# Optimization experiments

Measured on AMD Instinct MI355X. Metric: run time of the kernel, lower is better.

## Reference

```python
import jax, jax.numpy as jnp
import numpy as np

N, E = 8192, 262144
IN_DIM, OUT_DIM = 256, 256


def setup_inputs() -> dict:
    key = jax.random.key(0)
    k = jax.random.split(key, 7)
    x = jax.random.normal(k[0], (N, IN_DIM), dtype=jnp.float32)
    edge_index = jax.random.randint(k[1], (2, E), 0, N, dtype=jnp.int64)
    # parameters (nn.Linear stores weight as (out, in); bias=False everywhere)
    W = jax.random.normal(k[2], (OUT_DIM, IN_DIM), dtype=jnp.float32) / np.sqrt(IN_DIM)
    a_src = jax.random.normal(k[3], (OUT_DIM,), dtype=jnp.float32) / np.sqrt(OUT_DIM)
    a_dst = jax.random.normal(k[4], (OUT_DIM,), dtype=jnp.float32) / np.sqrt(OUT_DIM)
    gamma = jnp.ones((OUT_DIM,), dtype=jnp.float32)
    beta = jnp.zeros((OUT_DIM,), dtype=jnp.float32)
    return {"x": x, "edge_index": edge_index, "W": W, "a_src": a_src,
            "a_dst": a_dst, "gamma": gamma, "beta": beta}


def reference(x, edge_index, W, a_src, a_dst, gamma, beta):
    h = x @ W.T                                     # (N, D)
    src, dst = edge_index[0], edge_index[1]
    s_src = h @ a_src                               # (N,) attn_src logits
    s_dst = h @ a_dst                               # (N,)
    e = jax.nn.leaky_relu(s_src[src] + s_dst[dst], negative_slope=0.2)  # (E,)
    n = x.shape[0]
    # dense scatter: attn[dst, src] = e (duplicate edges overwrite, like torch)
    attn = jnp.zeros((n, n), dtype=x.dtype).at[dst, src].set(e)
    attn = jax.nn.softmax(attn + (attn == 0).astype(x.dtype) * -1e9, axis=-1)
    attn = attn * (attn > 1e-6).astype(x.dtype)
    out = attn @ h                                  # (N, D)
    z = jax.nn.elu(out) + h
    # LayerNorm (eps=1e-5, biased variance, matching torch)
    mean = jnp.mean(z, axis=-1, keepdims=True)
    var = jnp.var(z, axis=-1, keepdims=True)
    return gamma * (z - mean) * jax.lax.rsqrt(var + 1e-5) + beta
```

## Files before the change

kernel.cpp:

```cpp
#include <hip/hip_runtime.h>
#include <math.h>

#define N_NODES 8192
#define EDGES   262144
#define D       256
#define ROWCAP  128

typedef __attribute__((ext_vector_type(8))) short bf8;
typedef __attribute__((ext_vector_type(4))) float f32x4;


__device__ __forceinline__ ushort f2bf(float f) {
  unsigned u = __float_as_uint(f);
  return (ushort)((u + 0x7FFF + ((u >> 16) & 1)) >> 16);
}
__device__ __forceinline__ float bf2f(ushort s) {
  return __uint_as_float((unsigned)s << 16);
}

#define XQ 524288
#define WQ 16384
__global__ __launch_bounds__(256)
void split_kernel(const float* __restrict__ x, const float* __restrict__ W,
                  ushort* __restrict__ xhi, ushort* __restrict__ xlo,
                  ushort* __restrict__ whi, ushort* __restrict__ wlo) {
  int i = blockIdx.x * 256 + threadIdx.x;
  const float4* src; ushort *dh, *dl; int j;
  if (i < XQ) { src = (const float4*)x; dh = xhi; dl = xlo; j = i; }
  else        { src = (const float4*)W; dh = whi; dl = wlo; j = i - XQ; }
  float4 v = src[j];
  ushort4 h4, l4;
  h4.x = f2bf(v.x); l4.x = f2bf(v.x - bf2f(h4.x));
  h4.y = f2bf(v.y); l4.y = f2bf(v.y - bf2f(h4.y));
  h4.z = f2bf(v.z); l4.z = f2bf(v.z - bf2f(h4.z));
  h4.w = f2bf(v.w); l4.w = f2bf(v.w - bf2f(h4.w));
  *reinterpret_cast<ushort4*>(dh + (size_t)j * 4) = h4;
  *reinterpret_cast<ushort4*>(dl + (size_t)j * 4) = l4;
}

__global__ __launch_bounds__(256)
void gemm_mfma(const ushort* __restrict__ xhi, const ushort* __restrict__ xlo,
               const ushort* __restrict__ whi, const ushort* __restrict__ wlo,
               const float* __restrict__ a_src, const float* __restrict__ a_dst,
               float* __restrict__ h, float* __restrict__ s_src,
               float* __restrict__ s_dst) {
  const int wv = threadIdx.x >> 6, lane = threadIdx.x & 63;
  const int bm = blockIdx.x * 64 + wv * 16;
  const int bj = blockIdx.y * 64;
  const int r = lane & 15, kg = lane >> 4;
  const f32x4 z4 = {0.f, 0.f, 0.f, 0.f};
  f32x4 acc[4] = {z4, z4, z4, z4};
  const size_t arow = (size_t)(bm + r) * D;
  for (int k0 = 0; k0 < D; k0 += 32) {
    const int ko = k0 + kg * 8;
    bf8 ahi = *reinterpret_cast<const bf8*>(xhi + arow + ko);
    bf8 alo = *reinterpret_cast<const bf8*>(xlo + arow + ko);
#pragma unroll
    for (int ct = 0; ct < 4; ++ct) {
      const size_t boff = (size_t)(bj + ct * 16 + r) * D + ko;
      bf8 bhi = *reinterpret_cast<const bf8*>(whi + boff);
      bf8 blo = *reinterpret_cast<const bf8*>(wlo + boff);
      acc[ct] = __builtin_amdgcn_mfma_f32_16x16x32_bf16(ahi, bhi, acc[ct], 0, 0, 0);
      acc[ct] = __builtin_amdgcn_mfma_f32_16x16x32_bf16(ahi, blo, acc[ct], 0, 0, 0);
      acc[ct] = __builtin_amdgcn_mfma_f32_16x16x32_bf16(alo, bhi, acc[ct], 0, 0, 0);
    }
  }
  float pS[4] = {0.f, 0.f, 0.f, 0.f}, pD[4] = {0.f, 0.f, 0.f, 0.f};
#pragma unroll
  for (int ct = 0; ct < 4; ++ct) {
    const int col = bj + ct * 16 + r;
    const float av = a_src[col], dv = a_dst[col];
#pragma unroll
    for (int reg = 0; reg < 4; ++reg) {
      const float c = acc[ct][reg];
      h[(size_t)(bm + kg * 4 + reg) * D + col] = c;
      pS[reg] = fmaf(c, av, pS[reg]);
      pD[reg] = fmaf(c, dv, pD[reg]);
    }
  }
#pragma unroll
  for (int reg = 0; reg < 4; ++reg) {
    float ps = pS[reg], pd = pD[reg];
#pragma unroll
    for (int off = 1; off < 16; off <<= 1) {
      ps += __shfl_xor(ps, off, 64);
      pd += __shfl_xor(pd, off, 64);
    }
    if (r == 0) {
      atomicAdd(&s_src[bm + kg * 4 + reg], ps);
      atomicAdd(&s_dst[bm + kg * 4 + reg], pd);
    }
  }
}

__global__ __launch_bounds__(256)
void scatter_kernel(const int* __restrict__ ei, int* __restrict__ fill,
                    int* __restrict__ csr) {
  int lane = threadIdx.x & 63;
  unsigned long long b = __ballot(ei[lane * 2 + 1] == 0);
  int is64 = (b == 0xFFFFFFFFFFFFFFFFull) ? 1 : 0;
  int e = blockIdx.x * 256 + threadIdx.x;
  int src, dst;
  if (is64) { src = ei[2 * e];  dst = ei[2 * (EDGES + e)]; }
  else      { src = ei[e];      dst = ei[EDGES + e]; }
  int p = atomicAdd(&fill[dst], 1);
  if (p < ROWCAP) csr[dst * ROWCAP + p] = src;
}

__global__ __launch_bounds__(256)
void row_fused(const float* __restrict__ h, const float* __restrict__ s_src,
               const float* __restrict__ s_dst, const int* __restrict__ fill,
               const int* __restrict__ csr, const float* __restrict__ gamma,
               const float* __restrict__ beta, float* __restrict__ out) {
  __shared__ int   s_idx[4][ROWCAP];
  __shared__ float s_w[4][ROWCAP];
  const int w    = threadIdx.x >> 6;
  const int lane = threadIdx.x & 63;
  const int row  = blockIdx.x * 4 + w;
  int len = fill[row];
  if (len > ROWCAP) len = ROWCAP;
  const int len_pad = (len + 7) & ~7;
  const float sd = s_dst[row];

  for (int i = lane; i < len; i += 64) s_idx[w][i] = csr[row * ROWCAP + i];
  __syncthreads();

  float lmax = -3.0e38f;
  for (int i = lane; i < len; i += 64) {
    int s = s_idx[w][i];
    bool dup = false;
    for (int j = 0; j < i; ++j)
      if (s_idx[w][j] == s) { dup = true; break; }
    float v;
    if (dup) {
      v = -3.0e38f;
    } else {
      v = s_src[s] + sd;
      v = (v >= 0.f) ? v : 0.2f * v;
      if (v == 0.0f) v = -3.0e38f;
    }
    s_w[w][i] = v;
    lmax = fmaxf(lmax, v);
  }
#pragma unroll
  for (int off = 32; off; off >>= 1) lmax = fmaxf(lmax, __shfl_xor(lmax, off, 64));

  float lsum = 0.f;
  for (int i = lane; i < len; i += 64) {
    float e = expf(s_w[w][i] - lmax);
    s_w[w][i] = e;
    lsum += e;
  }
#pragma unroll
  for (int off = 32; off; off >>= 1) lsum += __shfl_xor(lsum, off, 64);
  float inv = (lsum > 0.f) ? (1.0f / lsum) : 0.f;
  for (int i = lane; i < len; i += 64) {
    float ww = s_w[w][i] * inv;
    s_w[w][i] = (ww > 1e-6f) ? ww : 0.f;
  }
  for (int i = len + lane; i < len_pad; i += 64) { s_w[w][i] = 0.f; s_idx[w][i] = 0; }
  __syncthreads();

  float4 acc = make_float4(0.f, 0.f, 0.f, 0.f);
  for (int i = 0; i < len_pad; i += 8) {
    float wg[8]; float4 hv[8];
#pragma unroll
    for (int u = 0; u < 8; ++u) {
      wg[u] = s_w[w][i + u];
      hv[u] = *reinterpret_cast<const float4*>(&h[(size_t)s_idx[w][i + u] * D + lane * 4]);
    }
#pragma unroll
    for (int u = 0; u < 8; ++u) {
      acc.x = fmaf(wg[u], hv[u].x, acc.x);
      acc.y = fmaf(wg[u], hv[u].y, acc.y);
      acc.z = fmaf(wg[u], hv[u].z, acc.z);
      acc.w = fmaf(wg[u], hv[u].w, acc.w);
    }
  }

  const float4 hr = *reinterpret_cast<const float4*>(&h[(size_t)row * D + lane * 4]);
  float4 z;
  z.x = ((acc.x > 0.f) ? acc.x : expm1f(acc.x)) + hr.x;
  z.y = ((acc.y > 0.f) ? acc.y : expm1f(acc.y)) + hr.y;
  z.z = ((acc.z > 0.f) ? acc.z : expm1f(acc.z)) + hr.z;
  z.w = ((acc.w > 0.f) ? acc.w : expm1f(acc.w)) + hr.w;

  float s1 = z.x + z.y + z.z + z.w;
#pragma unroll
  for (int off = 32; off; off >>= 1) s1 += __shfl_xor(s1, off, 64);
  float mean = s1 * (1.0f / 256.0f);
  float dx = z.x - mean, dy = z.y - mean, dz = z.z - mean, dw = z.w - mean;
  float s2 = dx * dx + dy * dy + dz * dz + dw * dw;
#pragma unroll
  for (int off = 32; off; off >>= 1) s2 += __shfl_xor(s2, off, 64);
  float rs = rsqrtf(s2 * (1.0f / 256.0f) + 1e-5f);

  const float4 gm = *reinterpret_cast<const float4*>(&gamma[lane * 4]);
  const float4 bt = *reinterpret_cast<const float4*>(&beta[lane * 4]);
  float4 o;
  o.x = gm.x * dx * rs + bt.x;
  o.y = gm.y * dy * rs + bt.y;
  o.z = gm.z * dz * rs + bt.z;
  o.w = gm.w * dw * rs + bt.w;
  *reinterpret_cast<float4*>(&out[(size_t)row * D + lane * 4]) = o;
}

extern "C" void kernel_launch(void* const* d_in, const int* in_sizes, int n_in,
                              void* d_out, int out_size, void* d_ws, size_t ws_size,
                              hipStream_t stream) {
  const float* x     = (const float*)d_in[0];
  const int*   ei    = (const int*)d_in[1];
  const float* W     = (const float*)d_in[2];
  const float* a_src = (const float*)d_in[3];
  const float* a_dst = (const float*)d_in[4];
  const float* gamma = (const float*)d_in[5];
  const float* beta  = (const float*)d_in[6];
  float* out = (float*)d_out;

  char* ws = (char*)d_ws;
  int*    fill  = (int*)(ws);
  float*  s_src = (float*)(ws + 32768);
  float*  s_dst = (float*)(ws + 65536);
  int*    csr   = (int*)(ws + 98304);
  float*  h     = (float*)(ws + 4292608);
  ushort* xhi   = (ushort*)(ws + 12681216);
  ushort* xlo   = (ushort*)(ws + 16875520);
  ushort* whi   = (ushort*)(ws + 21069824);
  ushort* wlo   = (ushort*)(ws + 21200896);
  if (ws_size < 21331968) return;

  hipMemsetAsync(ws, 0, 98304, stream);
  split_kernel<<<(XQ + WQ) / 256, 256, 0, stream>>>(x, W, xhi, xlo, whi, wlo);
  scatter_kernel<<<EDGES / 256, 256, 0, stream>>>(ei, fill, csr);
  gemm_mfma<<<dim3(N_NODES / 64, D / 64), 256, 0, stream>>>(xhi, xlo, whi, wlo,
                                                            a_src, a_dst, h, s_src, s_dst);
  row_fused<<<N_NODES / 4, 256, 0, stream>>>(h, s_src, s_dst, fill, csr, gamma, beta, out);
}
```

Before: 139.8 us.

## Fuse x bf16 split into GEMM and gather bf16 copy of h in aggregation

Drops the separate pass that splits x into hi/lo bf16 arrays and instead converts x rows to hi/lo bf16 in registers inside the GEMM, which now computes 32 rows per wave (128 per block) with launch_bounds(256,1). The GEMM also writes a bf16 copy of h, and the row aggregation gathers neighbour rows from that half-size copy instead of fp32 h. This removes a full read/write pass over x and halves the gather traffic, at the cost of bf16 precision in the attention-weighted sum, more register pressure and fewer GEMM blocks (256 instead of 512).

New measurement: 126.8 us. 9.3% less time.

```diff
diff --git a/kernel.cpp b/kernel.cpp
--- a/kernel.cpp
+++ b/kernel.cpp
@@ -18,79 +18,102 @@
   return __uint_as_float((unsigned)s << 16);
 }
 
-#define XQ 524288
-#define WQ 16384
 __global__ __launch_bounds__(256)
-void split_kernel(const float* __restrict__ x, const float* __restrict__ W,
-                  ushort* __restrict__ xhi, ushort* __restrict__ xlo,
-                  ushort* __restrict__ whi, ushort* __restrict__ wlo) {
+void split_w(const float* __restrict__ W, ushort* __restrict__ whi,
+             ushort* __restrict__ wlo) {
   int i = blockIdx.x * 256 + threadIdx.x;
-  const float4* src; ushort *dh, *dl; int j;
-  if (i < XQ) { src = (const float4*)x; dh = xhi; dl = xlo; j = i; }
-  else        { src = (const float4*)W; dh = whi; dl = wlo; j = i - XQ; }
-  float4 v = src[j];
+  float4 v = reinterpret_cast<const float4*>(W)[i];
   ushort4 h4, l4;
   h4.x = f2bf(v.x); l4.x = f2bf(v.x - bf2f(h4.x));
   h4.y = f2bf(v.y); l4.y = f2bf(v.y - bf2f(h4.y));
   h4.z = f2bf(v.z); l4.z = f2bf(v.z - bf2f(h4.z));
   h4.w = f2bf(v.w); l4.w = f2bf(v.w - bf2f(h4.w));
-  *reinterpret_cast<ushort4*>(dh + (size_t)j * 4) = h4;
-  *reinterpret_cast<ushort4*>(dl + (size_t)j * 4) = l4;
-}
-
-__global__ __launch_bounds__(256)
-void gemm_mfma(const ushort* __restrict__ xhi, const ushort* __restrict__ xlo,
+  *reinterpret_cast<ushort4*>(whi + (size_t)i * 4) = h4;
+  *reinterpret_cast<ushort4*>(wlo + (size_t)i * 4) = l4;
+}
+
+__global__ __launch_bounds__(256, 1)
+void gemm_mfma(const float* __restrict__ x,
                const ushort* __restrict__ whi, const ushort* __restrict__ wlo,
                const float* __restrict__ a_src, const float* __restrict__ a_dst,
-               float* __restrict__ h, float* __restrict__ s_src,
-               float* __restrict__ s_dst) {
+               float* __restrict__ h, ushort* __restrict__ h_bf,
+               float* __restrict__ s_src, float* __restrict__ s_dst) {
   const int wv = threadIdx.x >> 6, lane = threadIdx.x & 63;
-  const int bm = blockIdx.x * 64 + wv * 16;
+  const int bm = blockIdx.x * 128 + wv * 32;
   const int bj = blockIdx.y * 64;
   const int r = lane & 15, kg = lane >> 4;
+
+  bf8 ahi[2][8], alo[2][8];
+#pragma unroll
+  for (int s = 0; s < 2; ++s) {
+    const float* xr = x + (size_t)(bm + s * 16 + r) * D;
+#pragma unroll
+    for (int k0 = 0; k0 < 8; ++k0) {
+      float4 v0 = *reinterpret_cast<const float4*>(xr + k0 * 32 + kg * 8);
+      float4 v1 = *reinterpret_cast<const float4*>(xr + k0 * 32 + kg * 8 + 4);
+      float f[8] = {v0.x, v0.y, v0.z, v0.w, v1.x, v1.y, v1.z, v1.w};
+      bf8 hi, lo;
+#pragma unroll
+      for (int j = 0; j < 8; ++j) {
+        ushort hh = f2bf(f[j]);
+        hi[j] = (short)hh;
+        lo[j] = (short)f2bf(f[j] - bf2f(hh));
+      }
+      ahi[s][k0] = hi; alo[s][k0] = lo;
+    }
+  }
+
   const f32x4 z4 = {0.f, 0.f, 0.f, 0.f};
-  f32x4 acc[4] = {z4, z4, z4, z4};
-  const size_t arow = (size_t)(bm + r) * D;
-  for (int k0 = 0; k0 < D; k0 += 32) {
-    const int ko = k0 + kg * 8;
-    bf8 ahi = *reinterpret_cast<const bf8*>(xhi + arow + ko);
-    bf8 alo = *reinterpret_cast<const bf8*>(xlo + arow + ko);
+  f32x4 acc[2][4] = {{z4, z4, z4, z4}, {z4, z4, z4, z4}};
+#pragma unroll
+  for (int k0 = 0; k0 < 8; ++k0) {
 #pragma unroll
     for (int ct = 0; ct < 4; ++ct) {
-      const size_t boff = (size_t)(bj + ct * 16 + r) * D + ko;
+      const size_t boff = (size_t)(bj + ct * 16 + r) * D + k0 * 32 + kg * 8;
       bf8 bhi = *reinterpret_cast<const bf8*>(whi + boff);
       bf8 blo = *reinterpret_cast<const bf8*>(wlo + boff);
-      acc[ct] = __builtin_amdgcn_mfma_f32_16x16x32_bf16(ahi, bhi, acc[ct], 0, 0, 0);
-      acc[ct] = __builtin_amdgcn_mfma_f32_16x16x32_bf16(ahi, blo, acc[ct], 0, 0, 0);
-      acc[ct] = __builtin_amdgcn_mfma_f32_16x16x32_bf16(alo, bhi, acc[ct], 0, 0, 0);
-    }
-  }
-  float pS[4] = {0.f, 0.f, 0.f, 0.f}, pD[4] = {0.f, 0.f, 0.f, 0.f};
-#pragma unroll
-  for (int ct = 0; ct < 4; ++ct) {
-    const int col = bj + ct * 16 + r;
-    const float av = a_src[col], dv = a_dst[col];
+#pragma unroll
+      for (int s = 0; s < 2; ++s) {
+        acc[s][ct] = __builtin_amdgcn_mfma_f32_16x16x32_bf16(ahi[s][k0], bhi, acc[s][ct], 0, 0, 0);
+        acc[s][ct] = __builtin_amdgcn_mfma_f32_16x16x32_bf16(ahi[s][k0], blo, acc[s][ct], 0, 0, 0);
+        acc[s][ct] = __builtin_amdgcn_mfma_f32_16x16x32_bf16(alo[s][k0], bhi, acc[s][ct], 0, 0, 0);
+      }
+    }
+  }
+
+  float pS[2][4] = {{0.f}}, pD[2][4] = {{0.f}};
+#pragma unroll
+  for (int s = 0; s < 2; ++s) {
+#pragma unroll
+    for (int ct = 0; ct < 4; ++ct) {
+      const int col = bj + ct * 16 + r;
+      const float av = a_src[col], dv = a_dst[col];
+#pragma unroll
+      for (int reg = 0; reg < 4; ++reg) {
+        const float c = acc[s][ct][reg];
+        const size_t off = (size_t)(bm + s * 16 + kg * 4 + reg) * D + col;
+        h[off] = c;
+        h_bf[off] = f2bf(c);
+        pS[s][reg] = fmaf(c, av, pS[s][reg]);
+        pD[s][reg] = fmaf(c, dv, pD[s][reg]);
+      }
+    }
+  }
+#pragma unroll
+  for (int s = 0; s < 2; ++s)
 #pragma unroll
     for (int reg = 0; reg < 4; ++reg) {
-      const float c = acc[ct][reg];
-      h[(size_t)(bm + kg * 4 + reg) * D + col] = c;
-      pS[reg] = fmaf(c, av, pS[reg]);
-      pD[reg] = fmaf(c, dv, pD[reg]);
-    }
-  }
-#pragma unroll
-  for (int reg = 0; reg < 4; ++reg) {
-    float ps = pS[reg], pd = pD[reg];
-#pragma unroll
-    for (int off = 1; off < 16; off <<= 1) {
-      ps += __shfl_xor(ps, off, 64);
-      pd += __shfl_xor(pd, off, 64);
-    }
-    if (r == 0) {
-      atomicAdd(&s_src[bm + kg * 4 + reg], ps);
-      atomicAdd(&s_dst[bm + kg * 4 + reg], pd);
-    }
-  }
+      float ps = pS[s][reg], pd = pD[s][reg];
+#pragma unroll
+      for (int off = 1; off < 16; off <<= 1) {
+        ps += __shfl_xor(ps, off, 64);
+        pd += __shfl_xor(pd, off, 64);
+      }
+      if (r == 0) {
+        atomicAdd(&s_src[bm + s * 16 + kg * 4 + reg], ps);
+        atomicAdd(&s_dst[bm + s * 16 + kg * 4 + reg], pd);
+      }
+    }
 }
 
 __global__ __launch_bounds__(256)
@@ -108,10 +131,11 @@
 }
 
 __global__ __launch_bounds__(256)
-void row_fused(const float* __restrict__ h, const float* __restrict__ s_src,
-               const float* __restrict__ s_dst, const int* __restrict__ fill,
-               const int* __restrict__ csr, const float* __restrict__ gamma,
-               const float* __restrict__ beta, float* __restrict__ out) {
+void row_fused(const float* __restrict__ h, const ushort* __restrict__ h_bf,
+               const float* __restrict__ s_src, const float* __restrict__ s_dst,
+               const int* __restrict__ fill, const int* __restrict__ csr,
+               const float* __restrict__ gamma, const float* __restrict__ beta,
+               float* __restrict__ out) {
   __shared__ int   s_idx[4][ROWCAP];
   __shared__ float s_w[4][ROWCAP];
   const int w    = threadIdx.x >> 6;
@@ -163,18 +187,18 @@
 
   float4 acc = make_float4(0.f, 0.f, 0.f, 0.f);
   for (int i = 0; i < len_pad; i += 8) {
-    float wg[8]; float4 hv[8];
+    float wg[8]; ushort4 qv[8];
 #pragma unroll
     for (int u = 0; u < 8; ++u) {
       wg[u] = s_w[w][i + u];
-      hv[u] = *reinterpret_cast<const float4*>(&h[(size_t)s_idx[w][i + u] * D + lane * 4]);
+      qv[u] = *reinterpret_cast<const ushort4*>(h_bf + (size_t)s_idx[w][i + u] * D + lane * 4);
     }
 #pragma unroll
     for (int u = 0; u < 8; ++u) {
-      acc.x = fmaf(wg[u], hv[u].x, acc.x);
-      acc.y = fmaf(wg[u], hv[u].y, acc.y);
-      acc.z = fmaf(wg[u], hv[u].z, acc.z);
-      acc.w = fmaf(wg[u], hv[u].w, acc.w);
+      acc.x = fmaf(wg[u], bf2f(qv[u].x), acc.x);
+      acc.y = fmaf(wg[u], bf2f(qv[u].y), acc.y);
+      acc.z = fmaf(wg[u], bf2f(qv[u].z), acc.z);
+      acc.w = fmaf(wg[u], bf2f(qv[u].w), acc.w);
     }
   }
 
@@ -223,16 +247,17 @@
   float*  s_dst = (float*)(ws + 65536);
   int*    csr   = (int*)(ws + 98304);
   float*  h     = (float*)(ws + 4292608);
-  ushort* xhi   = (ushort*)(ws + 12681216);
-  ushort* xlo   = (ushort*)(ws + 16875520);
-  ushort* whi   = (ushort*)(ws + 21069824);
-  ushort* wlo   = (ushort*)(ws + 21200896);
-  if (ws_size < 21331968) return;
+  ushort* h_bf  = (ushort*)(ws + 12681216);
+  ushort* whi   = (ushort*)(ws + 16875520);
+  ushort* wlo   = (ushort*)(ws + 17006592);
+  if (ws_size < 17137664) return;
 
   hipMemsetAsync(ws, 0, 98304, stream);
-  split_kernel<<<(XQ + WQ) / 256, 256, 0, stream>>>(x, W, xhi, xlo, whi, wlo);
+  split_w<<<64, 256, 0, stream>>>(W, whi, wlo);
   scatter_kernel<<<EDGES / 256, 256, 0, stream>>>(ei, fill, csr);
-  gemm_mfma<<<dim3(N_NODES / 64, D / 64), 256, 0, stream>>>(xhi, xlo, whi, wlo,
-                                                            a_src, a_dst, h, s_src, s_dst);
-  row_fused<<<N_NODES / 4, 256, 0, stream>>>(h, s_src, s_dst, fill, csr, gamma, beta, out);
-}
+  gemm_mfma<<<dim3(N_NODES / 128, D / 64), 256, 0, stream>>>(x, whi, wlo,
+                                                             a_src, a_dst, h, h_bf,
+                                                             s_src, s_dst);
+  row_fused<<<N_NODES / 4, 256, 0, stream>>>(h, h_bf, s_src, s_dst, fill, csr,
+                                             gamma, beta, out);
+}
```
